# Kernel optimization log

Measured on AMD Instinct MI355X. Metric: run time of the kernel, lower is better.

Reference implementation:

```python
import jax, jax.numpy as jnp
import numpy as np

HEADS = 4
OUT_CH = 64
NEG_SLOPE = 0.2  # PyG GATConv default negative_slope


def setup_inputs() -> dict:
    key = jax.random.key(0)
    k1, k2, k3, k4, k5, k6 = jax.random.split(key, 6)
    N, E, IN_CH = 50000, 800000, 128
    x = jax.random.normal(k1, (N, IN_CH), dtype=jnp.float32)
    edge_index = jax.random.randint(k2, (2, E), 0, N, dtype=jnp.int64)
    # Learned parameters (glorot-style init)
    s_w = (6.0 / (IN_CH + HEADS * OUT_CH)) ** 0.5
    W = jax.random.uniform(k3, (IN_CH, HEADS * OUT_CH), minval=-s_w, maxval=s_w, dtype=jnp.float32)
    s_a = (6.0 / (1 + OUT_CH)) ** 0.5
    att_src = jax.random.uniform(k4, (HEADS, OUT_CH), minval=-s_a, maxval=s_a, dtype=jnp.float32)
    att_dst = jax.random.uniform(k5, (HEADS, OUT_CH), minval=-s_a, maxval=s_a, dtype=jnp.float32)
    bias = jnp.zeros((HEADS * OUT_CH,), dtype=jnp.float32)
    return {"x": x, "W": W, "att_src": att_src, "att_dst": att_dst, "bias": bias, "edge_index": edge_index}


def reference(x, W, att_src, att_dst, bias, edge_index):
    # Faithful GATConv (PyG defaults: add_self_loops=True, concat=True, eval mode => no dropout)
    N = x.shape[0]
    loops = jnp.arange(N, dtype=edge_index.dtype)
    src = jnp.concatenate([edge_index[0], loops])  # message source j
    dst = jnp.concatenate([edge_index[1], loops])  # message target i

    xp = (x @ W).reshape(N, HEADS, OUT_CH)          # [N, H, C]
    a_src = jnp.einsum('nhc,hc->nh', xp, att_src)   # [N, H]
    a_dst = jnp.einsum('nhc,hc->nh', xp, att_dst)   # [N, H]

    alpha = jax.nn.leaky_relu(a_src[src] + a_dst[dst], NEG_SLOPE)  # [E', H]
    # segment softmax over incoming edges of each target node
    amax = jax.ops.segment_max(alpha, dst, num_segments=N)
    ex = jnp.exp(alpha - jax.lax.stop_gradient(amax)[dst])
    denom = jax.ops.segment_sum(ex, dst, num_segments=N)
    coef = ex / denom[dst]                           # [E', H]

    msg = xp[src] * coef[:, :, None]                 # [E', H, C]
    out = jax.ops.segment_sum(msg, dst, num_segments=N)  # [N, H, C]
    return out.reshape(N, HEADS * OUT_CH) + bias
```

## Files before the change

### kernel.cpp

```cpp
#include <hip/hip_runtime.h>

#define HEADS 4
#define OUTC 64
#define INC 128
#define HC 256
#define NEG 0.2f

typedef __attribute__((ext_vector_type(8))) short bf16x8;
typedef __attribute__((ext_vector_type(4))) float f32x4;

static __device__ __forceinline__ float bf2f(unsigned short u){
  unsigned int x = ((unsigned int)u) << 16;
  return __uint_as_float(x);
}
static __device__ __forceinline__ unsigned short f2bf(float f){
  unsigned int x = __float_as_uint(f);
  unsigned int lsb = (x >> 16) & 1u;
  x += 0x7fffu + lsb;
  return (unsigned short)(x >> 16);
}
static __device__ __forceinline__ void split8(float4 a, float4 b, bf16x8& hi, bf16x8& lo){
  float v[8] = {a.x, a.y, a.z, a.w, b.x, b.y, b.z, b.w};
  #pragma unroll
  for (int i = 0; i < 8; ++i){
    unsigned short h = f2bf(v[i]);
    hi[i] = (short)h;
    lo[i] = (short)f2bf(v[i] - bf2f(h));
  }
}

#define SPLITB 128

__global__ void k_pre(const float* __restrict__ W, unsigned short* __restrict__ Wthi,
                      unsigned short* __restrict__ Wtlo, const int* __restrict__ ei,
                      int* __restrict__ srcc, int* __restrict__ dstc,
                      int* __restrict__ pos, int* __restrict__ deg, int E){
  if (blockIdx.x < SPLITB){
    int t = blockIdx.x * 256 + threadIdx.x;
    int k = t >> 8, n = t & 255;
    float v = W[t];
    unsigned short hi = f2bf(v);
    Wthi[n * INC + k] = hi;
    Wtlo[n * INC + k] = f2bf(v - bf2f(hi));
    return;
  }
  int e = (blockIdx.x - SPLITB) * 256 + threadIdx.x;
  bool valid = (e < E);
  int ee = valid ? e : 0;
  int hiw = ei[2 * ee + 1];
  bool hz = valid ? (hiw == 0) : true;
  unsigned long long mask = __ballot(hz);
  bool i64 = (mask == ~0ULL);
  int s, d;
  if (i64){ s = ei[2 * ee]; d = ei[2 * (size_t)E + 2 * ee]; }
  else    { s = ei[ee];     d = ei[(size_t)E + ee]; }
  if (valid){
    srcc[e] = s; dstc[e] = d;
    pos[e] = atomicAdd(&deg[d], 1);
  }
}

__global__ __launch_bounds__(256) void k_gemm_fused(const float* __restrict__ X,
    const unsigned short* __restrict__ Wthi, const unsigned short* __restrict__ Wtlo,
    const float* __restrict__ att_src, const float* __restrict__ att_dst,
    unsigned short* __restrict__ XPh, float* __restrict__ a_src, float* __restrict__ a_dst,
    int N){
  __shared__ unsigned short shi[64][40];
  __shared__ unsigned short slo[64][40];
  int w = threadIdx.x >> 6, lane = threadIdx.x & 63;
  int m0 = blockIdx.x * 64;
  int quad = lane >> 4;
  int l15 = lane & 15;
  int colg[4];
  #pragma unroll
  for (int t = 0; t < 4; ++t) colg[t] = w * 64 + t * 16 + l15;

  bool rv[4];
  #pragma unroll
  for (int rt = 0; rt < 4; ++rt) rv[rt] = (m0 + rt * 16) < N;
  int myrow = rv[w] ? (m0 + w * 16 + l15) : 0;

  f32x4 acc[4][4];
  #pragma unroll
  for (int rt = 0; rt < 4; ++rt)
    #pragma unroll
    for (int t = 0; t < 4; ++t) acc[rt][t] = (f32x4){0.f, 0.f, 0.f, 0.f};

  #pragma unroll
  for (int kk = 0; kk < 4; ++kk){
    const float* xr = X + (size_t)myrow * INC + kk * 32 + quad * 8;
    float4 va = *(const float4*)xr;
    float4 vb = *(const float4*)(xr + 4);
    bf16x8 bh[4], bl[4];
    #pragma unroll
    for (int t = 0; t < 4; ++t){
      size_t bo = (size_t)colg[t] * INC + kk * 32 + quad * 8;
      bh[t] = *(const bf16x8*)(Wthi + bo);
      bl[t] = *(const bf16x8*)(Wtlo + bo);
    }
    bf16x8 ah1, al1;
    split8(va, vb, ah1, al1);
    if (kk) __syncthreads();
    *(bf16x8*)&shi[w * 16 + l15][quad * 8] = ah1;
    *(bf16x8*)&slo[w * 16 + l15][quad * 8] = al1;
    __syncthreads();
    bf16x8 ah[4], al[4];
    #pragma unroll
    for (int rt = 0; rt < 4; ++rt){
      ah[rt] = *(const bf16x8*)&shi[rt * 16 + l15][quad * 8];
      al[rt] = *(const bf16x8*)&slo[rt * 16 + l15][quad * 8];
    }
    #pragma unroll
    for (int rt = 0; rt < 4; ++rt){
      #pragma unroll
      for (int t = 0; t < 4; ++t){
        acc[rt][t] = __builtin_amdgcn_mfma_f32_16x16x32_bf16(ah[rt], bh[t], acc[rt][t], 0, 0, 0);
        acc[rt][t] = __builtin_amdgcn_mfma_f32_16x16x32_bf16(ah[rt], bl[t], acc[rt][t], 0, 0, 0);
        acc[rt][t] = __builtin_amdgcn_mfma_f32_16x16x32_bf16(al[rt], bh[t], acc[rt][t], 0, 0, 0);
      }
    }
  }

  #pragma unroll
  for (int rt = 0; rt < 4; ++rt){
    if (!rv[rt]) continue;
    #pragma unroll
    for (int t = 0; t < 4; ++t){
      #pragma unroll
      for (int r = 0; r < 4; ++r){
        XPh[(size_t)(m0 + rt * 16 + quad * 4 + r) * HC + colg[t]] = f2bf(acc[rt][t][r]);
      }
    }
  }

  float as[4], ad[4];
  #pragma unroll
  for (int t = 0; t < 4; ++t){
    as[t] = att_src[colg[t]];
    ad[t] = att_dst[colg[t]];
  }
  #pragma unroll
  for (int rt = 0; rt < 4; ++rt){
    if (!rv[rt]) continue;
    float ps[4], pd[4];
    #pragma unroll
    for (int r = 0; r < 4; ++r){
      ps[r] = acc[rt][0][r] * as[0] + acc[rt][1][r] * as[1]
            + acc[rt][2][r] * as[2] + acc[rt][3][r] * as[3];
      pd[r] = acc[rt][0][r] * ad[0] + acc[rt][1][r] * ad[1]
            + acc[rt][2][r] * ad[2] + acc[rt][3][r] * ad[3];
    }
    #pragma unroll
    for (int msk = 1; msk < 16; msk <<= 1){
      #pragma unroll
      for (int r = 0; r < 4; ++r){
        ps[r] += __shfl_xor(ps[r], msk, 64);
        pd[r] += __shfl_xor(pd[r], msk, 64);
      }
    }
    if (l15 == 0){
      #pragma unroll
      for (int r = 0; r < 4; ++r){
        int n = m0 + rt * 16 + quad * 4 + r;
        a_src[n * HEADS + w] = ps[r];
        a_dst[n * HEADS + w] = pd[r];
      }
    }
  }
}

__global__ __launch_bounds__(256) void k_scan1(const int* __restrict__ deg,
                                               int* __restrict__ out,
                                               int* __restrict__ bsum, int N){
  __shared__ int tsum[256];
  int t = threadIdx.x;
  int base = blockIdx.x * 1024 + t * 4;
  int v[4]; int s = 0;
  #pragma unroll
  for (int k = 0; k < 4; ++k){ int i = base + k; v[k] = (i < N) ? deg[i] : 0; s += v[k]; }
  tsum[t] = s;
  __syncthreads();
  for (int off = 1; off < 256; off <<= 1){
    int x = (t >= off) ? tsum[t - off] : 0;
    __syncthreads();
    tsum[t] += x;
    __syncthreads();
  }
  int excl = tsum[t] - s;
  if (t == 255) bsum[blockIdx.x] = tsum[255];
  int run = excl;
  #pragma unroll
  for (int k = 0; k < 4; ++k){ int i = base + k; if (i < N) out[i] = run; run += v[k]; }
}

__global__ __launch_bounds__(256) void k_scan23(int* __restrict__ rowstart,
                                                const int* __restrict__ bsum,
                                                int N, int E){
  int lane = threadIdx.x & 63;
  int partial = 0;
  for (int i = lane; i < blockIdx.x; i += 64) partial += bsum[i];
  #pragma unroll
  for (int msk = 32; msk; msk >>= 1) partial += __shfl_xor(partial, msk, 64);
  int base = blockIdx.x * 1024 + threadIdx.x * 4;
  #pragma unroll
  for (int k = 0; k < 4; ++k){ int i = base + k; if (i < N) rowstart[i] += partial; }
  if (blockIdx.x == 0 && threadIdx.x == 0) rowstart[N] = E;
}

__global__ void k_scatter(const int* __restrict__ srcc, const int* __restrict__ dstc,
                          const int* __restrict__ pos, const int* __restrict__ rowstart,
                          int* __restrict__ csr, int E){
  int e = blockIdx.x * 256 + threadIdx.x;
  if (e < E){
    int d = dstc[e];
    csr[rowstart[d] + pos[e]] = srcc[e];
  }
}

__global__ __launch_bounds__(256) void k_fused(const unsigned short* __restrict__ XPh,
    const float* __restrict__ a_src, const float* __restrict__ a_dst,
    const int* __restrict__ rowstart, const int* __restrict__ csr,
    const float* __restrict__ bias, float* __restrict__ out, int N){
  __shared__ float sh[4][64][4];
  int w = threadIdx.x >> 6, lane = threadIdx.x & 63;
  int n = blockIdx.x * 4 + w;
  bool alive = (n < N);
  if (!alive) n = 0;
  int r0 = rowstart[n], r1 = rowstart[n + 1];
  int deg = r1 - r0;
  int total = deg + 1;
  int h = lane >> 4;
  float4 ad4 = *(const float4*)&a_dst[n * HEADS];
  bool fast = (total <= 64);
  int jv = n;
  float msel = 0.f, inv_sel = 0.f;

  if (fast){
    if (lane < deg) jv = csr[r0 + lane];
    float l0 = -1e30f, l1 = -1e30f, l2 = -1e30f, l3 = -1e30f;
    if (lane < total){
      float4 a4 = *(const float4*)&a_src[jv * HEADS];
      l0 = a4.x + ad4.x; l0 = (l0 > 0.f) ? l0 : NEG * l0;
      l1 = a4.y + ad4.y; l1 = (l1 > 0.f) ? l1 : NEG * l1;
      l2 = a4.z + ad4.z; l2 = (l2 > 0.f) ? l2 : NEG * l2;
      l3 = a4.w + ad4.w; l3 = (l3 > 0.f) ? l3 : NEG * l3;
    }
    float p0 = __expf(l0), p1 = __expf(l1), p2 = __expf(l2), p3 = __expf(l3);
    float s0 = p0, s1 = p1, s2 = p2, s3 = p3;
    #pragma unroll
    for (int msk = 32; msk; msk >>= 1){
      s0 += __shfl_xor(s0, msk, 64);
      s1 += __shfl_xor(s1, msk, 64);
      s2 += __shfl_xor(s2, msk, 64);
      s3 += __shfl_xor(s3, msk, 64);
    }
    if (lane < total){
      sh[w][lane][0] = p0 / s0;
      sh[w][lane][1] = p1 / s1;
      sh[w][lane][2] = p2 / s2;
      sh[w][lane][3] = p3 / s3;
    }
  } else {
    float m[4] = {-1e30f, -1e30f, -1e30f, -1e30f};
    float s[4] = {0.f, 0.f, 0.f, 0.f};
    float adArr[4] = {ad4.x, ad4.y, ad4.z, ad4.w};
    for (int e = lane; e < total; e += 64){
      int j = (e < deg) ? csr[r0 + e] : n;
      float4 a4 = *(const float4*)&a_src[j * HEADS];
      float aa[4] = {a4.x, a4.y, a4.z, a4.w};
      #pragma unroll
      for (int hh = 0; hh < 4; ++hh){
        float l = aa[hh] + adArr[hh];
        l = (l > 0.f) ? l : NEG * l;
        if (l > m[hh]){ s[hh] = s[hh] * __expf(m[hh] - l) + 1.f; m[hh] = l; }
        else            s[hh] += __expf(l - m[hh]);
      }
    }
    #pragma unroll
    for (int hh = 0; hh < 4; ++hh){
      float mm = m[hh], ss = s[hh];
      #pragma unroll
      for (int msk = 32; msk; msk >>= 1){
        float m2 = __shfl_xor(mm, msk, 64);
        float s2 = __shfl_xor(ss, msk, 64);
        float M = fmaxf(mm, m2);
        float ns = 0.f;
        if (mm > -1e29f) ns += ss * __expf(mm - M);
        if (m2 > -1e29f) ns += s2 * __expf(m2 - M);
        mm = M; ss = ns;
      }
      m[hh] = mm; s[hh] = ss;
    }
    msel    = (h == 0) ? m[0] : (h == 1) ? m[1] : (h == 2) ? m[2] : m[3];
    inv_sel = 1.f / ((h == 0) ? s[0] : (h == 1) ? s[1] : (h == 2) ? s[2] : s[3]);
  }

  float a0 = 0.f, a1 = 0.f, a2 = 0.f, a3 = 0.f;
  const unsigned short* xb = XPh + lane * 4;
  if (fast){
    int e = 0;
    for (; e + 8 <= total; e += 8){
      int jj[8]; float cf[8]; ushort4 xv[8];
      #pragma unroll
      for (int q = 0; q < 8; ++q){
        jj[q] = __builtin_amdgcn_readlane(jv, e + q);
        cf[q] = sh[w][e + q][h];
      }
      #pragma unroll
      for (int q = 0; q < 8; ++q) xv[q] = *(const ushort4*)(xb + (size_t)jj[q] * HC);
      #pragma unroll
      for (int q = 0; q < 8; ++q){
        a0 += cf[q] * bf2f(xv[q].x); a1 += cf[q] * bf2f(xv[q].y);
        a2 += cf[q] * bf2f(xv[q].z); a3 += cf[q] * bf2f(xv[q].w);
      }
    }
    for (; e < total; ++e){
      int j = __builtin_amdgcn_readlane(jv, e);
      float c = sh[w][e][h];
      ushort4 xv = *(const ushort4*)(xb + (size_t)j * HC);
      a0 += c * bf2f(xv.x); a1 += c * bf2f(xv.y); a2 += c * bf2f(xv.z); a3 += c * bf2f(xv.w);
    }
  } else {
    float adh = (h == 0) ? ad4.x : (h == 1) ? ad4.y : (h == 2) ? ad4.z : ad4.w;
    for (int e = 0; e < total; ++e){
      int j = (e < deg) ? csr[r0 + e] : n;
      float4 a4 = *(const float4*)&a_src[j * HEADS];
      float ah = (h == 0) ? a4.x : (h == 1) ? a4.y : (h == 2) ? a4.z : a4.w;
      float l = ah + adh;
      l = (l > 0.f) ? l : NEG * l;
      float c = __expf(l - msel) * inv_sel;
      ushort4 xv = *(const ushort4*)(xb + (size_t)j * HC);
      a0 += c * bf2f(xv.x); a1 += c * bf2f(xv.y); a2 += c * bf2f(xv.z); a3 += c * bf2f(xv.w);
    }
  }
  if (alive){
    float4 b4 = *(const float4*)&bias[lane * 4];
    f32x4 r;
    r[0] = a0 + b4.x; r[1] = a1 + b4.y; r[2] = a2 + b4.z; r[3] = a3 + b4.w;
    __builtin_nontemporal_store(r, (f32x4*)&out[(size_t)n * HC + lane * 4]);
  }
}

extern "C" void kernel_launch(void* const* d_in, const int* in_sizes, int n_in,
                              void* d_out, int out_size, void* d_ws, size_t ws_size,
                              hipStream_t stream){
  const float* x       = (const float*)d_in[0];
  const float* W       = (const float*)d_in[1];
  const float* att_src = (const float*)d_in[2];
  const float* att_dst = (const float*)d_in[3];
  const float* bias    = (const float*)d_in[4];
  const int*   ei      = (const int*)d_in[5];
  int N = in_sizes[0] / INC;
  int E = in_sizes[5] / 2;

  char* p = (char*)d_ws;
  auto alloc = [&](size_t bytes)->char*{
    char* r = p; p += (bytes + 255) & ~(size_t)255; return r;
  };
  unsigned short* Wthi = (unsigned short*)alloc((size_t)INC * HC * 2);
  unsigned short* Wtlo = (unsigned short*)alloc((size_t)INC * HC * 2);
  unsigned short* XPh  = (unsigned short*)alloc((size_t)N * HC * 2);
  float* aSrc          = (float*)alloc((size_t)N * HEADS * 4);
  float* aDst          = (float*)alloc((size_t)N * HEADS * 4);
  int* deg             = (int*)alloc((size_t)N * 4);
  int* rowstart        = (int*)alloc(((size_t)N + 1) * 4);
  int* srcc            = (int*)alloc((size_t)E * 4);
  int* dstc            = (int*)alloc((size_t)E * 4);
  int* pos             = (int*)alloc((size_t)E * 4);
  int* csr             = (int*)alloc((size_t)E * 4);
  int* bsum            = (int*)alloc(256 * 4);

  hipMemsetAsync(deg, 0, (size_t)N * 4, stream);
  k_pre<<<SPLITB + (E + 255) / 256, 256, 0, stream>>>(W, Wthi, Wtlo, ei,
                                                      srcc, dstc, pos, deg, E);
  k_gemm_fused<<<(N + 63) / 64, 256, 0, stream>>>(x, Wthi, Wtlo, att_src, att_dst,
                                                  XPh, aSrc, aDst, N);

  int nb = (N + 1023) / 1024;
  k_scan1<<<nb, 256, 0, stream>>>(deg, rowstart, bsum, N);
  k_scan23<<<nb, 256, 0, stream>>>(rowstart, bsum, N, E);
  k_scatter<<<(E + 255) / 256, 256, 0, stream>>>(srcc, dstc, pos, rowstart, csr, E);

  k_fused<<<(N + 3) / 4, 256, 0, stream>>>(XPh, aSrc, aDst, rowstart, csr, bias,
                                           (float*)d_out, N);
}
```

Measured before the change: 238.1 us.

## Fold degree scan into GEMM launch and compute block offsets in consumers

The per-block degree scan now runs as extra blocks of the GEMM kernel, so it overlaps with the projection and no longer needs its own launch. The separate add-block-offsets pass is removed: the scatter and aggregation kernels each rebuild the prefix of block sums in shared memory with a wavefront scan and add it on the fly. The aggregation kernel is also split into two launches over node halves. The intent is fewer dependent launches and less global traffic on the CSR build. The cost is redundant per-block prefix work, an assumption of at most 64 scan blocks, and one extra launch from the split.

```diff
diff --git a/kernel.cpp b/kernel.cpp
--- a/kernel.cpp
+++ b/kernel.cpp
@@ -60,13 +60,42 @@
   }
 }
 
-__global__ __launch_bounds__(256) void k_gemm_fused(const float* __restrict__ X,
+__global__ __launch_bounds__(256) void k_gemm_scan(const float* __restrict__ X,
     const unsigned short* __restrict__ Wthi, const unsigned short* __restrict__ Wtlo,
     const float* __restrict__ att_src, const float* __restrict__ att_dst,
     unsigned short* __restrict__ XPh, float* __restrict__ a_src, float* __restrict__ a_dst,
-    int N){
+    const int* __restrict__ deg, int* __restrict__ rowstart, int* __restrict__ bsum,
+    int N, int GB, int nb){
   __shared__ unsigned short shi[64][40];
   __shared__ unsigned short slo[64][40];
+  __shared__ int tsum[256];
+
+  if (blockIdx.x >= GB){
+    int sb = blockIdx.x - GB;
+    int t = threadIdx.x;
+    int base = sb * 1024 + t * 4;
+    int v[4]; int s = 0;
+    #pragma unroll
+    for (int k = 0; k < 4; ++k){ int i = base + k; v[k] = (i < N) ? deg[i] : 0; s += v[k]; }
+    tsum[t] = s;
+    __syncthreads();
+    for (int off = 1; off < 256; off <<= 1){
+      int x = (t >= off) ? tsum[t - off] : 0;
+      __syncthreads();
+      tsum[t] += x;
+      __syncthreads();
+    }
+    int excl = tsum[t] - s;
+    if (t == 255){
+      bsum[sb] = tsum[255];
+      if (sb == nb - 1) rowstart[N] = tsum[255];
+    }
+    int run = excl;
+    #pragma unroll
+    for (int k = 0; k < 4; ++k){ int i = base + k; if (i < N) rowstart[i] = run; run += v[k]; }
+    return;
+  }
+
   int w = threadIdx.x >> 6, lane = threadIdx.x & 63;
   int m0 = blockIdx.x * 64;
   int quad = lane >> 4;
@@ -169,64 +198,55 @@
   }
 }
 
-__global__ __launch_bounds__(256) void k_scan1(const int* __restrict__ deg,
-                                               int* __restrict__ out,
-                                               int* __restrict__ bsum, int N){
-  __shared__ int tsum[256];
+__global__ __launch_bounds__(256) void k_scatter(const int* __restrict__ srcc,
+                          const int* __restrict__ dstc, const int* __restrict__ pos,
+                          const int* __restrict__ rowstart, const int* __restrict__ bsum,
+                          int* __restrict__ csr, int E, int nb){
+  __shared__ int bps[65];
   int t = threadIdx.x;
-  int base = blockIdx.x * 1024 + t * 4;
-  int v[4]; int s = 0;
-  #pragma unroll
-  for (int k = 0; k < 4; ++k){ int i = base + k; v[k] = (i < N) ? deg[i] : 0; s += v[k]; }
-  tsum[t] = s;
+  if (t < 64){
+    int v = (t < nb) ? bsum[t] : 0;
+    #pragma unroll
+    for (int off = 1; off < 64; off <<= 1){
+      int u = __shfl_up(v, off, 64);
+      if (t >= off) v += u;
+    }
+    bps[t + 1] = v;
+    if (t == 0) bps[0] = 0;
+  }
   __syncthreads();
-  for (int off = 1; off < 256; off <<= 1){
-    int x = (t >= off) ? tsum[t - off] : 0;
-    __syncthreads();
-    tsum[t] += x;
-    __syncthreads();
-  }
-  int excl = tsum[t] - s;
-  if (t == 255) bsum[blockIdx.x] = tsum[255];
-  int run = excl;
-  #pragma unroll
-  for (int k = 0; k < 4; ++k){ int i = base + k; if (i < N) out[i] = run; run += v[k]; }
-}
-
-__global__ __launch_bounds__(256) void k_scan23(int* __restrict__ rowstart,
-                                                const int* __restrict__ bsum,
-                                                int N, int E){
-  int lane = threadIdx.x & 63;
-  int partial = 0;
-  for (int i = lane; i < blockIdx.x; i += 64) partial += bsum[i];
-  #pragma unroll
-  for (int msk = 32; msk; msk >>= 1) partial += __shfl_xor(partial, msk, 64);
-  int base = blockIdx.x * 1024 + threadIdx.x * 4;
-  #pragma unroll
-  for (int k = 0; k < 4; ++k){ int i = base + k; if (i < N) rowstart[i] += partial; }
-  if (blockIdx.x == 0 && threadIdx.x == 0) rowstart[N] = E;
-}
-
-__global__ void k_scatter(const int* __restrict__ srcc, const int* __restrict__ dstc,
-                          const int* __restrict__ pos, const int* __restrict__ rowstart,
-                          int* __restrict__ csr, int E){
-  int e = blockIdx.x * 256 + threadIdx.x;
+  int e = blockIdx.x * 256 + t;
   if (e < E){
     int d = dstc[e];
-    csr[rowstart[d] + pos[e]] = srcc[e];
+    csr[rowstart[d] + bps[d >> 10] + pos[e]] = srcc[e];
   }
 }
 
 __global__ __launch_bounds__(256) void k_fused(const unsigned short* __restrict__ XPh,
     const float* __restrict__ a_src, const float* __restrict__ a_dst,
-    const int* __restrict__ rowstart, const int* __restrict__ csr,
-    const float* __restrict__ bias, float* __restrict__ out, int N){
+    const int* __restrict__ rowstart, const int* __restrict__ bsum,
+    const int* __restrict__ csr, const float* __restrict__ bias,
+    float* __restrict__ out, int n0, int n1, int nb){
   __shared__ float sh[4][64][4];
+  __shared__ int bps[65];
   int w = threadIdx.x >> 6, lane = threadIdx.x & 63;
-  int n = blockIdx.x * 4 + w;
-  bool alive = (n < N);
-  if (!alive) n = 0;
-  int r0 = rowstart[n], r1 = rowstart[n + 1];
+  if (threadIdx.x < 64){
+    int v = (threadIdx.x < nb) ? bsum[threadIdx.x] : 0;
+    #pragma unroll
+    for (int off = 1; off < 64; off <<= 1){
+      int u = __shfl_up(v, off, 64);
+      if (threadIdx.x >= off) v += u;
+    }
+    bps[threadIdx.x + 1] = v;
+    if (threadIdx.x == 0) bps[0] = 0;
+  }
+  __syncthreads();
+
+  int n = n0 + blockIdx.x * 4 + w;
+  bool alive = (n < n1);
+  if (!alive) n = n0;
+  int r0 = rowstart[n] + bps[n >> 10];
+  int r1 = rowstart[n + 1] + bps[(n + 1) >> 10];
   int deg = r1 - r0;
   int total = deg + 1;
   int h = lane >> 4;
@@ -370,17 +390,21 @@
   int* csr             = (int*)alloc((size_t)E * 4);
   int* bsum            = (int*)alloc(256 * 4);
 
+  int GB = (N + 63) / 64;
+  int nb = (N + 1023) / 1024;
+
   hipMemsetAsync(deg, 0, (size_t)N * 4, stream);
   k_pre<<<SPLITB + (E + 255) / 256, 256, 0, stream>>>(W, Wthi, Wtlo, ei,
                                                       srcc, dstc, pos, deg, E);
-  k_gemm_fused<<<(N + 63) / 64, 256, 0, stream>>>(x, Wthi, Wtlo, att_src, att_dst,
-                                                  XPh, aSrc, aDst, N);
-
-  int nb = (N + 1023) / 1024;
-  k_scan1<<<nb, 256, 0, stream>>>(deg, rowstart, bsum, N);
-  k_scan23<<<nb, 256, 0, stream>>>(rowstart, bsum, N, E);
-  k_scatter<<<(E + 255) / 256, 256, 0, stream>>>(srcc, dstc, pos, rowstart, csr, E);
-
-  k_fused<<<(N + 3) / 4, 256, 0, stream>>>(XPh, aSrc, aDst, rowstart, csr, bias,
-                                           (float*)d_out, N);
-}
+  k_gemm_scan<<<GB + nb, 256, 0, stream>>>(x, Wthi, Wtlo, att_src, att_dst,
+                                           XPh, aSrc, aDst, deg, rowstart, bsum,
+                                           N, GB, nb);
+  k_scatter<<<(E + 255) / 256, 256, 0, stream>>>(srcc, dstc, pos, rowstart, bsum,
+                                                 csr, E, nb);
+
+  int Nh = ((N / 2) + 3) & ~3;
+  k_fused<<<(Nh + 3) / 4, 256, 0, stream>>>(XPh, aSrc, aDst, rowstart, bsum, csr,
+                                            bias, (float*)d_out, 0, Nh, nb);
+  k_fused<<<(N - Nh + 3) / 4, 256, 0, stream>>>(XPh, aSrc, aDst, rowstart, bsum, csr,
+                                                bias, (float*)d_out, Nh, N, nb);
+}
```

After: 242.0 us. About the same (+1.6%).
